# Optimization experiments

Hardware: AMD Instinct MI355X
Metric: run time of the kernel (lower is better)

The kernel has to match this reference:

```python
import jax, jax.numpy as jnp
import numpy as np

NEG = -1e9

def setup_inputs() -> dict:
    key = jax.random.key(0)
    kx, kq, kk, kv, kbq, kbk, kbv = jax.random.split(key, 7)
    B, S, E, D = 4, 2048, 1024, 64
    x = jax.random.normal(kx, (B, S, E), dtype=jnp.float32)
    # causal mask, broadcast over batch (mask == 0 positions get -1e9)
    mask = jnp.broadcast_to(jnp.tril(jnp.ones((S, S), dtype=jnp.int32)), (B, S, S))
    scale = 1.0 / np.sqrt(E)
    Wq = jax.random.normal(kq, (E, D), dtype=jnp.float32) * scale
    Wk = jax.random.normal(kk, (E, D), dtype=jnp.float32) * scale
    Wv = jax.random.normal(kv, (E, D), dtype=jnp.float32) * scale
    bq = jnp.zeros((D,), dtype=jnp.float32)
    bk = jnp.zeros((D,), dtype=jnp.float32)
    bv = jnp.zeros((D,), dtype=jnp.float32)
    return {"x": x, "mask": mask, "Wq": Wq, "bq": bq, "Wk": Wk, "bk": bk, "Wv": Wv, "bv": bv}

def reference(x, mask, Wq, bq, Wk, bk, Wv, bv):
    # Faithful to original: forward passes (K(x), Q(x), V(x)) into sdpa,
    # so the K-projection plays the 'query' role and Q-projection the 'key' role.
    q = jnp.einsum('bse,ed->bsd', x, Wk) + bk  # K(x) used as queries
    k = jnp.einsum('bse,ed->bsd', x, Wq) + bq  # Q(x) used as keys
    v = jnp.einsum('bse,ed->bsd', x, Wv) + bv
    d = q.shape[-1]
    scores = jnp.einsum('bsd,btd->bst', q, k) / jnp.sqrt(jnp.asarray(d, q.dtype))
    scores = jnp.where(mask == 0, jnp.asarray(NEG, scores.dtype), scores)
    weights = jax.nn.softmax(scores, axis=-1)
    return jnp.einsum('bst,btd->bsd', weights, v)
```

## Files before the change

kernel.cpp:

```cpp
#include <hip/hip_runtime.h>

typedef short bf16x8 __attribute__((ext_vector_type(8)));
typedef float f32x4  __attribute__((ext_vector_type(4)));
typedef int   i32x4  __attribute__((ext_vector_type(4)));

#define NEG_BIG (-1e9f)

__device__ __forceinline__ float bf2f(unsigned short h){
  union { unsigned u; float f; } v; v.u = ((unsigned)h) << 16; return v.f;
}
__device__ __forceinline__ unsigned short f2bf(float f){
  union { float f; unsigned u; } v; v.f = f;
  unsigned u = v.u;
  return (unsigned short)((u + 0x7FFFu + ((u >> 16) & 1u)) >> 16);
}
__device__ __forceinline__ void split1(float v, unsigned short& h, unsigned short& l){
  h = f2bf(v);
  l = f2bf(v - bf2f(h));
}
__device__ __forceinline__ void split_t(float v, unsigned short& h, unsigned short& l){
  union { float f; unsigned u; } c; c.f = v;
  h = (unsigned short)(c.u >> 16);
  union { unsigned u; float f; } hi; hi.u = c.u & 0xFFFF0000u;
  l = f2bf(v - hi.f);
}

__global__ __launch_bounds__(256) void prep_kernel(
    const float* __restrict__ Wq, const float* __restrict__ bq,
    const float* __restrict__ Wk, const float* __restrict__ bk,
    const float* __restrict__ Wv, const float* __restrict__ bv,
    unsigned short* __restrict__ Wimg, float* __restrict__ bias)
{
  int idx = blockIdx.x * 256 + threadIdx.x;
  if (idx < 192 * 1024) {
    int kb = idx / 6144, rem = idx % 6144;
    int r = rem >> 5, kk = rem & 31;
    int k = kb * 32 + kk;
    float v;
    if (r < 64)       v = Wk[k * 64 + r];
    else if (r < 128) v = Wq[k * 64 + (r - 64)];
    else              v = Wv[k * 64 + (r - 128)];
    unsigned short h, l; split1(v, h, l);
    Wimg[kb * 12288 + r * 64 + kk]      = h;
    Wimg[kb * 12288 + r * 64 + 32 + kk] = l;
  }
  if (idx < 192) {
    float b;
    if (idx < 64)       b = bk[idx];
    else if (idx < 128) b = bq[idx - 64];
    else                b = bv[idx - 128];
    bias[idx] = b;
  }
}

__global__ __launch_bounds__(256, 4) void proj_kernel(
    const float* __restrict__ x,
    const unsigned short* __restrict__ Wimg,
    const float* __restrict__ bias,
    unsigned short* __restrict__ Qh, unsigned short* __restrict__ Ql,
    unsigned short* __restrict__ Kh, unsigned short* __restrict__ Kl,
    unsigned short* __restrict__ Vth, unsigned short* __restrict__ Vtl)
{
  __shared__ __align__(16) float          Ax[32 * 32];
  __shared__ __align__(16) unsigned short Wc[96 * 64];

  const int tid  = threadIdx.x;
  const int lane = tid & 63;
  const int w    = tid >> 6;
  const int rh   = w & 1;
  const int cg   = w >> 1;
  const int quad = lane >> 4;
  const int li   = lane & 15;
  const int rowbase = (blockIdx.x >> 1) * 32;
  const int ch      = blockIdx.x & 1;

  const int ar = tid >> 3, ac = tid & 7;
  const float* agp = x + (size_t)(rowbase + ar) * 1024 + ac * 4;
  const int axslot = ar * 32 + (ac ^ (ar & 7)) * 4;
  int wr[3], whc[3], wslot[3];
  const unsigned short* wgp[3];
  #pragma unroll
  for (int j = 0; j < 3; j++) {
    int cid = tid + j * 256;
    wr[j]  = cid >> 3;
    whc[j] = cid & 7;
    wslot[j] = wr[j] * 64 + (whc[j] ^ (wr[j] & 7)) * 8;
    wgp[j] = Wimg + (size_t)(ch * 96 + wr[j]) * 64 + whc[j] * 8;
  }

  f32x4 acc[3];
  #pragma unroll
  for (int c = 0; c < 3; c++) acc[c] = (f32x4){0.f, 0.f, 0.f, 0.f};

  const int alr = rh * 16 + li;
  const int as0 = alr * 32 + ((2 * quad) ^ (li & 7)) * 4;
  const int as1 = alr * 32 + ((2 * quad + 1) ^ (li & 7)) * 4;

  f32x4 rA = *(const f32x4*)agp;
  i32x4 rW0 = *(const i32x4*)(wgp[0]);
  i32x4 rW1 = *(const i32x4*)(wgp[1]);
  i32x4 rW2 = *(const i32x4*)(wgp[2]);

  for (int kb = 0; kb < 32; kb++) {
    __syncthreads();
    *(f32x4*)&Ax[axslot] = rA;
    *(i32x4*)&Wc[wslot[0]] = rW0;
    *(i32x4*)&Wc[wslot[1]] = rW1;
    *(i32x4*)&Wc[wslot[2]] = rW2;
    if (kb < 31) {
      rA  = *(const f32x4*)(agp + (kb + 1) * 32);
      rW0 = *(const i32x4*)(wgp[0] + (size_t)(kb + 1) * 12288);
      rW1 = *(const i32x4*)(wgp[1] + (size_t)(kb + 1) * 12288);
      rW2 = *(const i32x4*)(wgp[2] + (size_t)(kb + 1) * 12288);
    }
    __syncthreads();

    f32x4 af0 = *(const f32x4*)&Ax[as0];
    f32x4 af1 = *(const f32x4*)&Ax[as1];
    bf16x8 ah, al;
    #pragma unroll
    for (int j = 0; j < 4; j++) {
      unsigned short h, l;
      split_t(af0[j], h, l); ah[j] = h;     al[j] = l;
      split_t(af1[j], h, l); ah[4+j] = h;   al[4+j] = l;
    }
    #pragma unroll
    for (int ct = 0; ct < 3; ct++) {
      const int lw = cg * 48 + ct * 16 + li;
      bf16x8 bh = *(const bf16x8*)&Wc[lw * 64 + (quad       ^ (li & 7)) * 8];
      bf16x8 bl = *(const bf16x8*)&Wc[lw * 64 + ((quad + 4) ^ (li & 7)) * 8];
      acc[ct] = __builtin_amdgcn_mfma_f32_16x16x32_bf16(ah, bh, acc[ct], 0, 0, 0);
      acc[ct] = __builtin_amdgcn_mfma_f32_16x16x32_bf16(al, bh, acc[ct], 0, 0, 0);
      acc[ct] = __builtin_amdgcn_mfma_f32_16x16x32_bf16(ah, bl, acc[ct], 0, 0, 0);
    }
  }

  #pragma unroll
  for (int ct = 0; ct < 3; ct++)
    #pragma unroll
    for (int r = 0; r < 4; r++) {
      int row = rowbase + rh * 16 + quad * 4 + r;
      int col = ch * 96 + cg * 48 + ct * 16 + li;
      float val = acc[ct][r] + bias[col];
      unsigned short h, l; split1(val, h, l);
      if (col < 64) {
        Qh[(size_t)row * 64 + col] = h;
        Ql[(size_t)row * 64 + col] = l;
      } else if (col < 128) {
        Kh[(size_t)row * 64 + (col - 64)] = h;
        Kl[(size_t)row * 64 + (col - 64)] = l;
      } else {
        int d = col - 128; int bb = row >> 11; int s = row & 2047;
        size_t o = (size_t)bb * 131072 + (size_t)d * 2048 + s;
        Vth[o] = h;
        Vtl[o] = l;
      }
    }
}

__global__ __launch_bounds__(512, 4) void attn_kernel(
    const unsigned short* __restrict__ Qh, const unsigned short* __restrict__ Ql,
    const unsigned short* __restrict__ Kh, const unsigned short* __restrict__ Kl,
    const unsigned short* __restrict__ Vth, const unsigned short* __restrict__ Vtl,
    float* __restrict__ out)
{
  __shared__ __align__(16) char smem[8 * 4096];
  __shared__ float ml_l[8][16];

  const int tid  = threadIdx.x;
  const int w    = tid >> 6;
  const int lane = tid & 63;
  const int quad = lane >> 4;
  const int li   = lane & 15;
  const int b    = blockIdx.x & 3;
  const int qt   = 127 - (blockIdx.x >> 2);
  const int qbase = qt * 16;
  const int nkt  = (qbase >> 6) + 1;

  unsigned short* p_s  = (unsigned short*)(smem + w * 4096);
  float*          lacc = (float*)(smem + w * 4096);

  size_t qoff = ((size_t)(b * 2048 + qbase) + li) * 64 + quad * 8;
  bf16x8 qh0 = *(const bf16x8*)(Qh + qoff);
  bf16x8 qh1 = *(const bf16x8*)(Qh + qoff + 32);
  bf16x8 ql0 = *(const bf16x8*)(Ql + qoff);
  bf16x8 ql1 = *(const bf16x8*)(Ql + qoff + 32);

  f32x4 acc_o[4];
  #pragma unroll
  for (int c = 0; c < 4; c++) acc_o[c] = (f32x4){0.f, 0.f, 0.f, 0.f};
  float l[4] = {0.f, 0.f, 0.f, 0.f};

  for (int kt = w; kt < nkt; kt += 8) {
    const int kb = kt * 64;
    f32x4 s[4];
    #pragma unroll
    for (int c = 0; c < 4; c++) s[c] = (f32x4){0.f, 0.f, 0.f, 0.f};

    #pragma unroll
    for (int ct = 0; ct < 4; ct++) {
      size_t ko = (size_t)(b * 2048 + kb + ct * 16 + li) * 64 + quad * 8;
      bf16x8 kh0 = *(const bf16x8*)(Kh + ko);
      bf16x8 kh1 = *(const bf16x8*)(Kh + ko + 32);
      bf16x8 kl0 = *(const bf16x8*)(Kl + ko);
      bf16x8 kl1 = *(const bf16x8*)(Kl + ko + 32);
      s[ct] = __builtin_amdgcn_mfma_f32_16x16x32_bf16(qh0, kh0, s[ct], 0, 0, 0);
      s[ct] = __builtin_amdgcn_mfma_f32_16x16x32_bf16(qh1, kh1, s[ct], 0, 0, 0);
      s[ct] = __builtin_amdgcn_mfma_f32_16x16x32_bf16(ql0, kh0, s[ct], 0, 0, 0);
      s[ct] = __builtin_amdgcn_mfma_f32_16x16x32_bf16(ql1, kh1, s[ct], 0, 0, 0);
      s[ct] = __builtin_amdgcn_mfma_f32_16x16x32_bf16(qh0, kl0, s[ct], 0, 0, 0);
      s[ct] = __builtin_amdgcn_mfma_f32_16x16x32_bf16(qh1, kl1, s[ct], 0, 0, 0);
    }

    {
      const bool diag = (kt == nkt - 1);
      float psum[4] = {0.f, 0.f, 0.f, 0.f};
      #pragma unroll
      for (int ct = 0; ct < 4; ct++)
        #pragma unroll
        for (int r = 0; r < 4; r++) {
          float v = s[ct][r] * 0.125f;
          if (diag && (kb + ct * 16 + li > qbase + quad * 4 + r)) v = NEG_BIG;
          float e = __expf(v - 16.0f);
          s[ct][r] = e;
          psum[r] += e;
        }
      #pragma unroll
      for (int off = 1; off < 16; off <<= 1)
        #pragma unroll
        for (int r = 0; r < 4; r++)
          psum[r] += __shfl_xor(psum[r], off, 64);
      #pragma unroll
      for (int r = 0; r < 4; r++) l[r] += psum[r];
      #pragma unroll
      for (int ct = 0; ct < 4; ct++)
        #pragma unroll
        for (int r = 0; r < 4; r++)
          p_s[(quad * 4 + r) * 72 + ct * 16 + li] = f2bf(s[ct][r]);
    }
    bf16x8 ap0 = *(const bf16x8*)&p_s[li * 72 + quad * 8];
    bf16x8 ap1 = *(const bf16x8*)&p_s[li * 72 + 32 + quad * 8];

    #pragma unroll
    for (int ct = 0; ct < 4; ct++) {
      size_t vo = (size_t)b * 131072 + (size_t)(ct * 16 + li) * 2048 + kb + quad * 8;
      bf16x8 vh0 = *(const bf16x8*)(Vth + vo);
      bf16x8 vh1 = *(const bf16x8*)(Vth + vo + 32);
      bf16x8 vl0 = *(const bf16x8*)(Vtl + vo);
      bf16x8 vl1 = *(const bf16x8*)(Vtl + vo + 32);
      acc_o[ct] = __builtin_amdgcn_mfma_f32_16x16x32_bf16(ap0, vh0, acc_o[ct], 0, 0, 0);
      acc_o[ct] = __builtin_amdgcn_mfma_f32_16x16x32_bf16(ap1, vh1, acc_o[ct], 0, 0, 0);
      acc_o[ct] = __builtin_amdgcn_mfma_f32_16x16x32_bf16(ap0, vl0, acc_o[ct], 0, 0, 0);
      acc_o[ct] = __builtin_amdgcn_mfma_f32_16x16x32_bf16(ap1, vl1, acc_o[ct], 0, 0, 0);
    }
  }

  if (li == 0) {
    #pragma unroll
    for (int r = 0; r < 4; r++)
      ml_l[w][quad * 4 + r] = l[r];
  }
  #pragma unroll
  for (int ct = 0; ct < 4; ct++)
    #pragma unroll
    for (int r = 0; r < 4; r++)
      lacc[(quad * 4 + r) * 64 + ct * 16 + li] = acc_o[ct][r];
  __syncthreads();

  {
    int row = tid >> 5;
    int c0  = (tid & 31) * 2;
    float s0 = 0.f, s1 = 0.f, L = 0.f;
    #pragma unroll
    for (int j = 0; j < 8; j++) {
      const float* lj = (const float*)(smem + j * 4096);
      s0 += lj[row * 64 + c0];
      s1 += lj[row * 64 + c0 + 1];
      L  += ml_l[j][row];
    }
    float inv = 1.f / L;
    size_t o = ((size_t)(b * 2048 + qbase + row)) * 64 + c0;
    out[o]     = s0 * inv;
    out[o + 1] = s1 * inv;
  }
}

extern "C" void kernel_launch(void* const* d_in, const int* in_sizes, int n_in,
                              void* d_out, int out_size, void* d_ws, size_t ws_size,
                              hipStream_t stream)
{
  (void)in_sizes; (void)n_in; (void)out_size; (void)ws_size;
  const float* x  = (const float*)d_in[0];
  const float* Wq = (const float*)d_in[2];
  const float* bq = (const float*)d_in[3];
  const float* Wk = (const float*)d_in[4];
  const float* bk = (const float*)d_in[5];
  const float* Wv = (const float*)d_in[6];
  const float* bv = (const float*)d_in[7];
  float* out = (float*)d_out;

  char* ws = (char*)d_ws;
  const size_t MB = 1u << 20;
  unsigned short* Qh   = (unsigned short*)(ws);
  unsigned short* Ql   = (unsigned short*)(ws + 1 * MB);
  unsigned short* Kh   = (unsigned short*)(ws + 2 * MB);
  unsigned short* Kl   = (unsigned short*)(ws + 3 * MB);
  unsigned short* Vth  = (unsigned short*)(ws + 4 * MB);
  unsigned short* Vtl  = (unsigned short*)(ws + 5 * MB);
  unsigned short* Wimg = (unsigned short*)(ws + 6 * MB);
  float*          bias = (float*)(ws + 6 * MB + 786432);

  prep_kernel<<<dim3(768), dim3(256), 0, stream>>>(Wq, bq, Wk, bk, Wv, bv, Wimg, bias);
  proj_kernel<<<dim3(512), dim3(256), 0, stream>>>(x, Wimg, bias, Qh, Ql, Kh, Kl, Vth, Vtl);
  attn_kernel<<<dim3(512), dim3(512), 0, stream>>>(Qh, Ql, Kh, Kl, Vth, Vtl, out);
}
```

Baseline: 185.7 us.

## Restructure attention into LDS-tiled split-K partial kernel plus merge, drop K/V low parts

Reworks attention so each 256-thread block handles 64 query rows and stages 64x64 K and V tiles in swizzled shared memory, prefetching the next tile in registers. All four waves reuse each tile instead of every wave reading K and V from global memory. Long causal rows are split across two blocks whose partial sums are combined by a new merge kernel. The low bf16 parts of K and V are dropped, which cuts MFMA count and memory traffic but lowers precision, and it adds an extra launch, partial-result traffic and only 192 blocks of parallelism.

```diff
diff --git a/kernel.cpp b/kernel.cpp
--- a/kernel.cpp
+++ b/kernel.cpp
@@ -58,8 +58,7 @@
     const unsigned short* __restrict__ Wimg,
     const float* __restrict__ bias,
     unsigned short* __restrict__ Qh, unsigned short* __restrict__ Ql,
-    unsigned short* __restrict__ Kh, unsigned short* __restrict__ Kl,
-    unsigned short* __restrict__ Vth, unsigned short* __restrict__ Vtl)
+    unsigned short* __restrict__ Kh, unsigned short* __restrict__ Vth)
 {
   __shared__ __align__(16) float          Ax[32 * 32];
   __shared__ __align__(16) unsigned short Wc[96 * 64];
@@ -148,37 +147,45 @@
         Ql[(size_t)row * 64 + col] = l;
       } else if (col < 128) {
         Kh[(size_t)row * 64 + (col - 64)] = h;
-        Kl[(size_t)row * 64 + (col - 64)] = l;
       } else {
         int d = col - 128; int bb = row >> 11; int s = row & 2047;
-        size_t o = (size_t)bb * 131072 + (size_t)d * 2048 + s;
-        Vth[o] = h;
-        Vtl[o] = l;
+        Vth[(size_t)bb * 131072 + (size_t)d * 2048 + s] = h;
       }
     }
 }
 
-__global__ __launch_bounds__(512, 4) void attn_kernel(
+__global__ __launch_bounds__(256, 2) void attn_part_kernel(
     const unsigned short* __restrict__ Qh, const unsigned short* __restrict__ Ql,
-    const unsigned short* __restrict__ Kh, const unsigned short* __restrict__ Kl,
-    const unsigned short* __restrict__ Vth, const unsigned short* __restrict__ Vtl,
-    float* __restrict__ out)
-{
-  __shared__ __align__(16) char smem[8 * 4096];
-  __shared__ float ml_l[8][16];
+    const unsigned short* __restrict__ Kh, const unsigned short* __restrict__ Vth,
+    float* __restrict__ pacc, float* __restrict__ pl)
+{
+  __shared__ __align__(16) unsigned short Kst[64 * 64];
+  __shared__ __align__(16) unsigned short Vst[64 * 64];
+  __shared__ __align__(16) unsigned short Ps[4][16 * 72];
 
   const int tid  = threadIdx.x;
+  const int lane = tid & 63;
   const int w    = tid >> 6;
-  const int lane = tid & 63;
   const int quad = lane >> 4;
   const int li   = lane & 15;
-  const int b    = blockIdx.x & 3;
-  const int qt   = 127 - (blockIdx.x >> 2);
-  const int qbase = qt * 16;
-  const int nkt  = (qbase >> 6) + 1;
-
-  unsigned short* p_s  = (unsigned short*)(smem + w * 4096);
-  float*          lacc = (float*)(smem + w * 4096);
+
+  const int id = blockIdx.x;
+  const int b  = id / 48;
+  const int r48 = id % 48;
+  int qg, part, kt0, kt1;
+  if (r48 < 32) {
+    qg = 31 - (r48 >> 1);
+    part = r48 & 1;
+    int nkt = qg + 1, h = (nkt + 1) >> 1;
+    kt0 = part ? h : 0;
+    kt1 = part ? nkt : h;
+  } else {
+    qg = 47 - r48;
+    part = 0;
+    kt0 = 0;
+    kt1 = qg + 1;
+  }
+  const int qbase = qg * 64 + w * 16;
 
   size_t qoff = ((size_t)(b * 2048 + qbase) + li) * 64 + quad * 8;
   bf16x8 qh0 = *(const bf16x8*)(Qh + qoff);
@@ -186,103 +193,135 @@
   bf16x8 ql0 = *(const bf16x8*)(Ql + qoff);
   bf16x8 ql1 = *(const bf16x8*)(Ql + qoff + 32);
 
-  f32x4 acc_o[4];
-  #pragma unroll
-  for (int c = 0; c < 4; c++) acc_o[c] = (f32x4){0.f, 0.f, 0.f, 0.f};
+  f32x4 acc[4];
+  #pragma unroll
+  for (int c = 0; c < 4; c++) acc[c] = (f32x4){0.f, 0.f, 0.f, 0.f};
   float l[4] = {0.f, 0.f, 0.f, 0.f};
 
-  for (int kt = w; kt < nkt; kt += 8) {
-    const int kb = kt * 64;
+  const int srow = tid >> 2, sc = tid & 3;
+  const unsigned short* kgp = Kh + (size_t)(b * 2048 + srow) * 64 + sc * 8;
+  const unsigned short* vgp = Vth + (size_t)b * 131072 + (size_t)srow * 2048 + sc * 8;
+  const int ks0 = srow * 64 + ((sc)     ^ (srow & 7)) * 8;
+  const int ks1 = srow * 64 + ((sc + 4) ^ (srow & 7)) * 8;
+
+  i32x4 rk0 = *(const i32x4*)(kgp + (size_t)kt0 * 4096);
+  i32x4 rk1 = *(const i32x4*)(kgp + (size_t)kt0 * 4096 + 32);
+  i32x4 rv0 = *(const i32x4*)(vgp + kt0 * 64);
+  i32x4 rv1 = *(const i32x4*)(vgp + kt0 * 64 + 32);
+
+  for (int kt = kt0; kt < kt1; kt++) {
+    __syncthreads();
+    *(i32x4*)&Kst[ks0] = rk0;
+    *(i32x4*)&Kst[ks1] = rk1;
+    *(i32x4*)&Vst[ks0] = rv0;
+    *(i32x4*)&Vst[ks1] = rv1;
+    if (kt + 1 < kt1) {
+      rk0 = *(const i32x4*)(kgp + (size_t)(kt + 1) * 4096);
+      rk1 = *(const i32x4*)(kgp + (size_t)(kt + 1) * 4096 + 32);
+      rv0 = *(const i32x4*)(vgp + (kt + 1) * 64);
+      rv1 = *(const i32x4*)(vgp + (kt + 1) * 64 + 32);
+    }
+    __syncthreads();
+
     f32x4 s[4];
     #pragma unroll
     for (int c = 0; c < 4; c++) s[c] = (f32x4){0.f, 0.f, 0.f, 0.f};
-
     #pragma unroll
     for (int ct = 0; ct < 4; ct++) {
-      size_t ko = (size_t)(b * 2048 + kb + ct * 16 + li) * 64 + quad * 8;
-      bf16x8 kh0 = *(const bf16x8*)(Kh + ko);
-      bf16x8 kh1 = *(const bf16x8*)(Kh + ko + 32);
-      bf16x8 kl0 = *(const bf16x8*)(Kl + ko);
-      bf16x8 kl1 = *(const bf16x8*)(Kl + ko + 32);
+      const int n = ct * 16 + li;
+      bf16x8 kh0 = *(const bf16x8*)&Kst[n * 64 + ((quad)     ^ (n & 7)) * 8];
+      bf16x8 kh1 = *(const bf16x8*)&Kst[n * 64 + ((quad + 4) ^ (n & 7)) * 8];
       s[ct] = __builtin_amdgcn_mfma_f32_16x16x32_bf16(qh0, kh0, s[ct], 0, 0, 0);
       s[ct] = __builtin_amdgcn_mfma_f32_16x16x32_bf16(qh1, kh1, s[ct], 0, 0, 0);
       s[ct] = __builtin_amdgcn_mfma_f32_16x16x32_bf16(ql0, kh0, s[ct], 0, 0, 0);
       s[ct] = __builtin_amdgcn_mfma_f32_16x16x32_bf16(ql1, kh1, s[ct], 0, 0, 0);
-      s[ct] = __builtin_amdgcn_mfma_f32_16x16x32_bf16(qh0, kl0, s[ct], 0, 0, 0);
-      s[ct] = __builtin_amdgcn_mfma_f32_16x16x32_bf16(qh1, kl1, s[ct], 0, 0, 0);
     }
 
     {
-      const bool diag = (kt == nkt - 1);
+      const bool diag = (kt == qg);
+      const int kb = kt * 64;
       float psum[4] = {0.f, 0.f, 0.f, 0.f};
       #pragma unroll
       for (int ct = 0; ct < 4; ct++)
         #pragma unroll
-        for (int r = 0; r < 4; r++) {
-          float v = s[ct][r] * 0.125f;
-          if (diag && (kb + ct * 16 + li > qbase + quad * 4 + r)) v = NEG_BIG;
+        for (int rr = 0; rr < 4; rr++) {
+          float v = s[ct][rr] * 0.125f;
+          if (diag && (kb + ct * 16 + li > qbase + quad * 4 + rr)) v = NEG_BIG;
           float e = __expf(v - 16.0f);
-          s[ct][r] = e;
-          psum[r] += e;
+          s[ct][rr] = e;
+          psum[rr] += e;
         }
       #pragma unroll
       for (int off = 1; off < 16; off <<= 1)
         #pragma unroll
-        for (int r = 0; r < 4; r++)
-          psum[r] += __shfl_xor(psum[r], off, 64);
+        for (int rr = 0; rr < 4; rr++)
+          psum[rr] += __shfl_xor(psum[rr], off, 64);
       #pragma unroll
-      for (int r = 0; r < 4; r++) l[r] += psum[r];
+      for (int rr = 0; rr < 4; rr++) l[rr] += psum[rr];
       #pragma unroll
       for (int ct = 0; ct < 4; ct++)
         #pragma unroll
-        for (int r = 0; r < 4; r++)
-          p_s[(quad * 4 + r) * 72 + ct * 16 + li] = f2bf(s[ct][r]);
-    }
-    bf16x8 ap0 = *(const bf16x8*)&p_s[li * 72 + quad * 8];
-    bf16x8 ap1 = *(const bf16x8*)&p_s[li * 72 + 32 + quad * 8];
+        for (int rr = 0; rr < 4; rr++)
+          Ps[w][(quad * 4 + rr) * 72 + ct * 16 + li] = f2bf(s[ct][rr]);
+    }
+    bf16x8 ap0 = *(const bf16x8*)&Ps[w][li * 72 + quad * 8];
+    bf16x8 ap1 = *(const bf16x8*)&Ps[w][li * 72 + 32 + quad * 8];
 
     #pragma unroll
     for (int ct = 0; ct < 4; ct++) {
-      size_t vo = (size_t)b * 131072 + (size_t)(ct * 16 + li) * 2048 + kb + quad * 8;
-      bf16x8 vh0 = *(const bf16x8*)(Vth + vo);
-      bf16x8 vh1 = *(const bf16x8*)(Vth + vo + 32);
-      bf16x8 vl0 = *(const bf16x8*)(Vtl + vo);
-      bf16x8 vl1 = *(const bf16x8*)(Vtl + vo + 32);
-      acc_o[ct] = __builtin_amdgcn_mfma_f32_16x16x32_bf16(ap0, vh0, acc_o[ct], 0, 0, 0);
-      acc_o[ct] = __builtin_amdgcn_mfma_f32_16x16x32_bf16(ap1, vh1, acc_o[ct], 0, 0, 0);
-      acc_o[ct] = __builtin_amdgcn_mfma_f32_16x16x32_bf16(ap0, vl0, acc_o[ct], 0, 0, 0);
-      acc_o[ct] = __builtin_amdgcn_mfma_f32_16x16x32_bf16(ap1, vl1, acc_o[ct], 0, 0, 0);
-    }
-  }
-
+      const int n = ct * 16 + li;
+      bf16x8 vh0 = *(const bf16x8*)&Vst[n * 64 + ((quad)     ^ (n & 7)) * 8];
+      bf16x8 vh1 = *(const bf16x8*)&Vst[n * 64 + ((quad + 4) ^ (n & 7)) * 8];
+      acc[ct] = __builtin_amdgcn_mfma_f32_16x16x32_bf16(ap0, vh0, acc[ct], 0, 0, 0);
+      acc[ct] = __builtin_amdgcn_mfma_f32_16x16x32_bf16(ap1, vh1, acc[ct], 0, 0, 0);
+    }
+  }
+
+  const int slot = (b * 32 + qg) * 2 + part;
+  float* pa = pacc + (size_t)slot * 4096;
+  #pragma unroll
+  for (int ct = 0; ct < 4; ct++)
+    #pragma unroll
+    for (int rr = 0; rr < 4; rr++)
+      pa[(w * 16 + quad * 4 + rr) * 64 + ct * 16 + li] = acc[ct][rr];
   if (li == 0) {
     #pragma unroll
-    for (int r = 0; r < 4; r++)
-      ml_l[w][quad * 4 + r] = l[r];
-  }
-  #pragma unroll
-  for (int ct = 0; ct < 4; ct++)
-    #pragma unroll
-    for (int r = 0; r < 4; r++)
-      lacc[(quad * 4 + r) * 64 + ct * 16 + li] = acc_o[ct][r];
-  __syncthreads();
-
-  {
-    int row = tid >> 5;
-    int c0  = (tid & 31) * 2;
-    float s0 = 0.f, s1 = 0.f, L = 0.f;
-    #pragma unroll
-    for (int j = 0; j < 8; j++) {
-      const float* lj = (const float*)(smem + j * 4096);
-      s0 += lj[row * 64 + c0];
-      s1 += lj[row * 64 + c0 + 1];
-      L  += ml_l[j][row];
-    }
-    float inv = 1.f / L;
-    size_t o = ((size_t)(b * 2048 + qbase + row)) * 64 + c0;
-    out[o]     = s0 * inv;
-    out[o + 1] = s1 * inv;
-  }
+    for (int rr = 0; rr < 4; rr++)
+      pl[slot * 64 + w * 16 + quad * 4 + rr] = l[rr];
+  }
+}
+
+__global__ __launch_bounds__(256) void attn_merge_kernel(
+    const float* __restrict__ pacc, const float* __restrict__ pl,
+    float* __restrict__ out)
+{
+  const int tid = threadIdx.x;
+  const int b   = blockIdx.x >> 5;
+  const int qg  = blockIdx.x & 31;
+  const int rr  = tid >> 2;
+  const int c0  = (tid & 3) * 16;
+  const int slot0 = (b * 32 + qg) * 2;
+
+  const float* pa0 = pacc + (size_t)slot0 * 4096 + rr * 64 + c0;
+  f32x4 a0 = *(const f32x4*)(pa0);
+  f32x4 a1 = *(const f32x4*)(pa0 + 4);
+  f32x4 a2 = *(const f32x4*)(pa0 + 8);
+  f32x4 a3 = *(const f32x4*)(pa0 + 12);
+  float L = pl[slot0 * 64 + rr];
+  if (qg >= 16) {
+    const float* pa1 = pacc + (size_t)(slot0 + 1) * 4096 + rr * 64 + c0;
+    a0 += *(const f32x4*)(pa1);
+    a1 += *(const f32x4*)(pa1 + 4);
+    a2 += *(const f32x4*)(pa1 + 8);
+    a3 += *(const f32x4*)(pa1 + 12);
+    L += pl[(slot0 + 1) * 64 + rr];
+  }
+  float inv = 1.f / L;
+  float* o = out + ((size_t)(b * 2048 + qg * 64 + rr)) * 64 + c0;
+  *(f32x4*)(o)      = a0 * inv;
+  *(f32x4*)(o + 4)  = a1 * inv;
+  *(f32x4*)(o + 8)  = a2 * inv;
+  *(f32x4*)(o + 12) = a3 * inv;
 }
 
 extern "C" void kernel_launch(void* const* d_in, const int* in_sizes, int n_in,
@@ -304,13 +343,14 @@
   unsigned short* Qh   = (unsigned short*)(ws);
   unsigned short* Ql   = (unsigned short*)(ws + 1 * MB);
   unsigned short* Kh   = (unsigned short*)(ws + 2 * MB);
-  unsigned short* Kl   = (unsigned short*)(ws + 3 * MB);
   unsigned short* Vth  = (unsigned short*)(ws + 4 * MB);
-  unsigned short* Vtl  = (unsigned short*)(ws + 5 * MB);
   unsigned short* Wimg = (unsigned short*)(ws + 6 * MB);
   float*          bias = (float*)(ws + 6 * MB + 786432);
+  float*          pacc = (float*)(ws + 8 * MB);
+  float*          pl   = (float*)(ws + 12 * MB);
 
   prep_kernel<<<dim3(768), dim3(256), 0, stream>>>(Wq, bq, Wk, bk, Wv, bv, Wimg, bias);
-  proj_kernel<<<dim3(512), dim3(256), 0, stream>>>(x, Wimg, bias, Qh, Ql, Kh, Kl, Vth, Vtl);
-  attn_kernel<<<dim3(512), dim3(512), 0, stream>>>(Qh, Ql, Kh, Kl, Vth, Vtl, out);
-}
+  proj_kernel<<<dim3(512), dim3(256), 0, stream>>>(x, Wimg, bias, Qh, Ql, Kh, Vth);
+  attn_part_kernel<<<dim3(192), dim3(256), 0, stream>>>(Qh, Ql, Kh, Vth, pacc, pl);
+  attn_merge_kernel<<<dim3(128), dim3(256), 0, stream>>>(pacc, pl, out);
+}
```

Result: faster. 162.5 us (-12.5%).
